# Optimization experiments

Measured on AMD Instinct MI355X. Metric: run time of the kernel, lower is better.

Reference implementation:

```python
import jax, jax.numpy as jnp
import numpy as np

NEG_INF = -(2.0**32) + 1.0  # matches tf: -2**32 + 1


def _positional_encoding(seq_len, d_model):
    # sinusoidal PE exactly as in the module (sin on even cols, cos on odd cols)
    pos = np.arange(seq_len)[:, None].astype(np.float32)
    i = np.arange(d_model)[None, :]
    angle_rates = 1.0 / np.power(10000.0, 2 * (i // 2) / np.float32(d_model))
    ang = pos * angle_rates
    ang[:, 0::2] = np.sin(ang[:, 0::2])
    ang[:, 1::2] = np.cos(ang[:, 1::2])
    return jnp.asarray(ang[None, ...], dtype=jnp.float32)  # [1, S, D]


def setup_inputs() -> dict:
    key = jax.random.key(0)
    kq, kk, kv, kw, km = jax.random.split(key, 5)
    B, S, D = 64, 512, 256
    q = jax.random.normal(kq, (B, S, D), dtype=jnp.float32)
    k = jax.random.normal(kk, (B, S, D), dtype=jnp.float32)
    v = jax.random.normal(kv, (B, S, D), dtype=jnp.float32)
    # keras 'random_uniform' initializer default range is [-0.05, 0.05]
    W = jax.random.uniform(kw, (D, D), dtype=jnp.float32, minval=-0.05, maxval=0.05)
    mask = jax.random.randint(km, (B, S), 0, 2, dtype=jnp.int32)
    return {"q": q, "k": k, "v": v, "W": W, "mask": mask}


def reference(q, k, v, W, mask):
    B, S, D = q.shape
    pe = _positional_encoding(S, D)  # [1, S, D]
    q = q + pe
    k = k + pe
    q = jax.nn.relu(jnp.einsum('bsd,de->bse', q, W))
    k = jax.nn.relu(jnp.einsum('bsd,de->bse', k, W))
    logits = jnp.einsum('bqd,bkd->bqk', q, k) / jnp.sqrt(jnp.float32(D))  # [B,S,S]
    # mask over key positions, broadcast across query dim
    logits = jnp.where(mask[:, None, :] == 0, jnp.float32(NEG_INF), logits)
    att = jax.nn.softmax(logits, axis=-1)
    out = jnp.einsum('bqk,bkd->bqd', att, v)
    return jnp.mean(out, axis=1)  # [B, D]
```

## Files before the change

### kernel.cpp

```cpp
#include <hip/hip_runtime.h>

#define NEG_INF (-4294967295.0f)

typedef _Float16 f16;
typedef _Float16 f16x8 __attribute__((ext_vector_type(8)));
typedef _Float16 f16x4v __attribute__((ext_vector_type(4)));
typedef float f32x4 __attribute__((ext_vector_type(4)));

#define MFMA16(a,b,c) __builtin_amdgcn_mfma_f32_16x16x32_f16((a),(b),(c),0,0,0)

#if defined(__has_builtin)
#if __has_builtin(__builtin_amdgcn_global_load_lds)
#define HAS_GLD 1
#endif
#endif

__device__ __forceinline__ void stage16(const void* g, void* lds_base, int lane) {
#ifdef HAS_GLD
    __builtin_amdgcn_global_load_lds(
        (const __attribute__((address_space(1))) unsigned int*)g,
        (__attribute__((address_space(3))) unsigned int*)lds_base, 16, 0, 0);
#else
    ((f16x8*)lds_base)[lane] = *(const f16x8*)g;
#endif
}

__global__ __launch_bounds__(256) void setup_kernel(const float* __restrict__ W,
                                                    float* __restrict__ pe,
                                                    f16* __restrict__ WT,
                                                    float* __restrict__ WG,
                                                    float* __restrict__ out) {
    const int bid = blockIdx.x, t = threadIdx.x;
    if (bid < 512) {
        int idx = bid * 256 + t;
        int s = idx >> 8, d = idx & 255;
        float x = (float)(d & ~1) * (1.f / 256.f);
        float rate = exp2f(x * -13.287712379549449f);
        float ang = (float)s * rate;
        pe[idx] = (d & 1) ? cosf(ang) : sinf(ang);
    } else if (bid < 768) {
        int e = bid - 512, d = t;
        WT[(e << 8) + d] = (f16)W[(d << 8) + e];
    } else if (bid == 768) {
        #pragma unroll
        for (int i = 0; i < 128; ++i) WG[i * 256 + t] = 0.f;
    } else {
        #pragma unroll
        for (int i = 0; i < 64; ++i) out[i * 256 + t] = 0.f;
    }
}

__global__ __launch_bounds__(1024, 4) void proj_kernel(const float* __restrict__ q,
                                                       const float* __restrict__ k,
                                                       const f16* __restrict__ WT,
                                                       const float* __restrict__ pe,
                                                       f16* __restrict__ outp) {
    __shared__ __align__(16) f16 lds[65536];
    f16* const As0 = lds;
    f16* const As1 = lds + 16384;
    f16* const Ws0 = lds + 32768;
    f16* const Ws1 = lds + 49152;

    const int t = threadIdx.x, l = t & 63, wv = t >> 6, lr = l & 15, lg = l >> 4;
    const int r0 = blockIdx.x * 256;
    const float* src = (r0 < 32768) ? q : k;
    const int rb = r0 & 32767;

    float4 av[4], pv[4];
    auto loadA = [&](int kc) {
        #pragma unroll
        for (int it = 0; it < 4; ++it) {
            int r = it * 64 + (t >> 4), d = (t & 15) * 4;
            av[it] = *(const float4*)(src + (size_t)(rb + r) * 256 + kc * 64 + d);
            pv[it] = *(const float4*)(pe + ((rb + r) & 511) * 256 + kc * 64 + d);
        }
    };
    auto writeA = [&](f16* dst) {
        #pragma unroll
        for (int it = 0; it < 4; ++it) {
            int r = it * 64 + (t >> 4), d = (t & 15) * 4;
            f16x4v h;
            h[0] = (f16)(av[it].x + pv[it].x); h[1] = (f16)(av[it].y + pv[it].y);
            h[2] = (f16)(av[it].z + pv[it].z); h[3] = (f16)(av[it].w + pv[it].w);
            *(f16x4v*)&dst[(r << 6) + (d ^ ((r & 7) << 3))] = h;
        }
    };
    auto stageW = [&](f16* dst, int kc) {
        #pragma unroll
        for (int it = 0; it < 2; ++it) {
            int eb = wv * 16 + it * 8;
            int e = eb + (l >> 3), c = l & 7;
            const f16* s = WT + (e << 8) + kc * 64 + ((c ^ (e & 7)) << 3);
            stage16(s, &dst[eb << 6], l);
        }
    };

    f32x4 acc[16] = {};
    loadA(0); stageW(Ws0, 0); writeA(As0);
    __syncthreads();

    #pragma unroll
    for (int kc = 0; kc < 4; ++kc) {
        f16* const Ac = (kc & 1) ? As1 : As0;
        f16* const Wc = (kc & 1) ? Ws1 : Ws0;
        f16* const An = (kc & 1) ? As0 : As1;
        f16* const Wn = (kc & 1) ? Ws0 : Ws1;
        if (kc < 3) { loadA(kc + 1); stageW(Wn, kc + 1); }
        #pragma unroll
        for (int kk = 0; kk < 2; ++kk) {
            int dk = kk * 32 + lg * 8;
            f16x8 a = *(const f16x8*)&Ac[((wv * 16 + lr) << 6) + (dk ^ ((lr & 7) << 3))];
            #pragma unroll
            for (int nt = 0; nt < 16; ++nt) {
                int e = nt * 16 + lr;
                f16x8 b = *(const f16x8*)&Wc[(e << 6) + (dk ^ ((lr & 7) << 3))];
                acc[nt] = MFMA16(a, b, acc[nt]);
            }
        }
        if (kc < 3) { writeA(An); __syncthreads(); }
    }

    __syncthreads();
    f16* Rb = lds + wv * 4096;
    #pragma unroll
    for (int nt = 0; nt < 16; ++nt) {
        #pragma unroll
        for (int rg = 0; rg < 4; ++rg) {
            int rr = lg * 4 + rg, col = nt * 16 + lr;
            float v = acc[nt][rg];
            v = v > 0.f ? v * 0.25f : 0.f;
            Rb[rr * 256 + ((((col >> 3) ^ (rr & 7)) << 3) | (col & 7))] = (f16)v;
        }
    }
    #pragma unroll
    for (int it = 0; it < 8; ++it) {
        int row = it * 2 + (l >> 5), c = l & 31;
        f16x8 v8 = *(const f16x8*)&Rb[row * 256 + ((c ^ (row & 7)) << 3)];
        *(f16x8*)(outp + (((size_t)(r0 + wv * 16 + row)) << 8) + c * 8) = v8;
    }
}

__global__ __launch_bounds__(256) void attn_kernel(const f16* __restrict__ QP,
                                                   const f16* __restrict__ KP,
                                                   const int* __restrict__ mask,
                                                   float* __restrict__ wglob) {
    __shared__ __align__(16) f16 Ks[2][32 * 256];
    __shared__ float ws[4][512];
    const int t = threadIdx.x, l = t & 63, wv = t >> 6, lr = l & 15, lg = l >> 4;
    const int n = blockIdx.x, bb = n & 63, qt = n >> 6;
    const int q0 = qt * 64 + wv * 16;
    const int* maskb = mask + bb * 512;

    auto stageK = [&](int dst, int kt) {
        #pragma unroll
        for (int it = 0; it < 4; ++it) {
            int r2 = wv * 8 + it * 2;
            int r = r2 + (l >> 5), c = l & 31;
            const f16* s = KP + (((size_t)(bb * 512 + kt * 32 + r)) << 8) + ((c ^ (r & 7)) << 3);
            stage16(s, &Ks[dst][r2 << 8], l);
        }
    };

    f16x8 qf[8];
    const f16* qrow = QP + (((size_t)(bb * 512 + q0 + lr)) << 8);
    #pragma unroll
    for (int kk = 0; kk < 8; ++kk) qf[kk] = *(const f16x8*)(qrow + kk * 32 + lg * 8);

    unsigned mb0 = 0, mb1 = 0;
    #pragma unroll
    for (int kt = 0; kt < 16; ++kt) {
        mb0 |= (maskb[kt * 32 + lr] ? 1u : 0u) << kt;
        mb1 |= (maskb[kt * 32 + 16 + lr] ? 1u : 0u) << kt;
    }

    float lacc[4] = {0.f, 0.f, 0.f, 0.f};
    f16 Pst[16][8];

    stageK(0, 0);
    __syncthreads();

    #pragma unroll
    for (int kt = 0; kt < 16; ++kt) {
        const int cur = kt & 1;
        if (kt < 15) stageK(cur ^ 1, kt + 1);
        f32x4 s0 = {}, s1 = {};
        #pragma unroll
        for (int kk = 0; kk < 8; ++kk) {
            int dk = kk * 32 + lg * 8;
            f16x8 b0 = *(const f16x8*)&Ks[cur][(lr << 8) + (dk ^ ((lr & 7) << 3))];
            f16x8 b1 = *(const f16x8*)&Ks[cur][((16 + lr) << 8) + (dk ^ ((lr & 7) << 3))];
            s0 = MFMA16(qf[kk], b0, s0);
            s1 = MFMA16(qf[kk], b1, s1);
        }
        #pragma unroll
        for (int rg = 0; rg < 4; ++rg) {
            float p0 = __expf(((mb0 >> kt) & 1) ? s0[rg] : NEG_INF);
            float p1 = __expf(((mb1 >> kt) & 1) ? s1[rg] : NEG_INF);
            f16 h0 = (f16)p0, h1 = (f16)p1;
            Pst[kt][rg] = h0;
            Pst[kt][4 + rg] = h1;
            lacc[rg] += (float)h0 + (float)h1;
        }
        if (kt < 15) __syncthreads();
    }

    #pragma unroll
    for (int rg = 0; rg < 4; ++rg) {
        float s = lacc[rg];
        s += __shfl_xor(s, 1); s += __shfl_xor(s, 2);
        s += __shfl_xor(s, 4); s += __shfl_xor(s, 8);
        lacc[rg] = s;
    }
    float rl[4];
    float bsum = 0.f;
    #pragma unroll
    for (int rg = 0; rg < 4; ++rg) {
        if (lacc[rg] > 0.f) { rl[rg] = 1.0f / lacc[rg]; }
        else                { rl[rg] = 0.f; bsum += 1.f / 512.f; }
    }

    #pragma unroll
    for (int kt = 0; kt < 16; ++kt) {
        float w0 = (float)Pst[kt][0] * rl[0] + (float)Pst[kt][1] * rl[1]
                 + (float)Pst[kt][2] * rl[2] + (float)Pst[kt][3] * rl[3] + bsum;
        float w1 = (float)Pst[kt][4] * rl[0] + (float)Pst[kt][5] * rl[1]
                 + (float)Pst[kt][6] * rl[2] + (float)Pst[kt][7] * rl[3] + bsum;
        w0 += __shfl_xor(w0, 16); w0 += __shfl_xor(w0, 32);
        w1 += __shfl_xor(w1, 16); w1 += __shfl_xor(w1, 32);
        if (lg == 0) {
            ws[wv][kt * 32 + lr] = w0;
            ws[wv][kt * 32 + 16 + lr] = w1;
        }
    }
    __syncthreads();
    #pragma unroll
    for (int i = 0; i < 2; ++i) {
        int kk = t + i * 256;
        float s = ws[0][kk] + ws[1][kk] + ws[2][kk] + ws[3][kk];
        atomicAdd(&wglob[bb * 512 + kk], s);
    }
}

__global__ __launch_bounds__(256) void wv_kernel(const float* __restrict__ wglob,
                                                 const float* __restrict__ V,
                                                 float* __restrict__ out) {
    const int n = blockIdx.x, bb = n & 63, ks = n >> 6;
    const int d = threadIdx.x;
    const float* wr = wglob + bb * 512 + ks * 64;
    const float* vb = V + ((((size_t)bb) * 512 + ks * 64) << 8) + d;
    float acc = 0.f;
    #pragma unroll 8
    for (int kk = 0; kk < 64; ++kk) acc = fmaf(wr[kk], vb[(size_t)kk << 8], acc);
    atomicAdd(&out[bb * 256 + d], acc * (1.f / 512.f));
}

extern "C" void kernel_launch(void* const* d_in, const int* in_sizes, int n_in,
                              void* d_out, int out_size, void* d_ws, size_t ws_size,
                              hipStream_t stream) {
    const float* q  = (const float*)d_in[0];
    const float* k  = (const float*)d_in[1];
    const float* v  = (const float*)d_in[2];
    const float* W  = (const float*)d_in[3];
    const int* mask = (const int*)d_in[4];

    char* ws = (char*)d_ws;
    f16*   QP = (f16*)ws;
    f16*   KP = (f16*)(ws + 16777216);
    float* PE = (float*)(ws + 33554432);
    f16*   WT = (f16*)(ws + 34078720);
    float* WG = (float*)(ws + 34209792);

    setup_kernel<<<770, 256, 0, stream>>>(W, PE, WT, WG, (float*)d_out);
    proj_kernel<<<256, 1024, 0, stream>>>(q, k, WT, PE, QP);
    attn_kernel<<<512, 256, 0, stream>>>(QP, KP, mask, WG);
    wv_kernel<<<512, 256, 0, stream>>>(WG, v, (float*)d_out);
}
```

Measured before the change: 175.9 us.

## Shrink projection blocks and keep A fragments in registers instead of LDS

The projection kernel moves from 1024-thread blocks covering 256 rows to 256-thread blocks covering 64 rows, launched as 1024 blocks. Each wave now loads its 16 input rows plus positional encoding straight into f16 register fragments for the whole K dimension. Only W is staged through a single 32 KB LDS buffer, replacing the earlier double-buffered A and W tiles. The aim is to cut LDS use and per-block size so more blocks fit per CU and more work runs in parallel. The cost is losing the double-buffered overlap of W loads (there is now a sync before and after each chunk), W being re-staged four times as often across the grid, and higher register pressure from the eight A fragments.

```diff
diff --git a/kernel.cpp b/kernel.cpp
--- a/kernel.cpp
+++ b/kernel.cpp
@@ -4,7 +4,6 @@
 
 typedef _Float16 f16;
 typedef _Float16 f16x8 __attribute__((ext_vector_type(8)));
-typedef _Float16 f16x4v __attribute__((ext_vector_type(4)));
 typedef float f32x4 __attribute__((ext_vector_type(4)));
 
 #define MFMA16(a,b,c) __builtin_amdgcn_mfma_f32_16x16x32_f16((a),(b),(c),0,0,0)
@@ -50,78 +49,61 @@
     }
 }
 
-__global__ __launch_bounds__(1024, 4) void proj_kernel(const float* __restrict__ q,
-                                                       const float* __restrict__ k,
-                                                       const f16* __restrict__ WT,
-                                                       const float* __restrict__ pe,
-                                                       f16* __restrict__ outp) {
-    __shared__ __align__(16) f16 lds[65536];
-    f16* const As0 = lds;
-    f16* const As1 = lds + 16384;
-    f16* const Ws0 = lds + 32768;
-    f16* const Ws1 = lds + 49152;
-
+__global__ __launch_bounds__(256, 4) void proj_kernel(const float* __restrict__ q,
+                                                      const float* __restrict__ k,
+                                                      const f16* __restrict__ WT,
+                                                      const float* __restrict__ pe,
+                                                      f16* __restrict__ outp) {
+    __shared__ __align__(16) f16 Ws[256 * 64];
     const int t = threadIdx.x, l = t & 63, wv = t >> 6, lr = l & 15, lg = l >> 4;
-    const int r0 = blockIdx.x * 256;
+    const int r0 = blockIdx.x * 64;
     const float* src = (r0 < 32768) ? q : k;
     const int rb = r0 & 32767;
 
-    float4 av[4], pv[4];
-    auto loadA = [&](int kc) {
-        #pragma unroll
-        for (int it = 0; it < 4; ++it) {
-            int r = it * 64 + (t >> 4), d = (t & 15) * 4;
-            av[it] = *(const float4*)(src + (size_t)(rb + r) * 256 + kc * 64 + d);
-            pv[it] = *(const float4*)(pe + ((rb + r) & 511) * 256 + kc * 64 + d);
-        }
-    };
-    auto writeA = [&](f16* dst) {
-        #pragma unroll
-        for (int it = 0; it < 4; ++it) {
-            int r = it * 64 + (t >> 4), d = (t & 15) * 4;
-            f16x4v h;
-            h[0] = (f16)(av[it].x + pv[it].x); h[1] = (f16)(av[it].y + pv[it].y);
-            h[2] = (f16)(av[it].z + pv[it].z); h[3] = (f16)(av[it].w + pv[it].w);
-            *(f16x4v*)&dst[(r << 6) + (d ^ ((r & 7) << 3))] = h;
-        }
-    };
-    auto stageW = [&](f16* dst, int kc) {
-        #pragma unroll
-        for (int it = 0; it < 2; ++it) {
-            int eb = wv * 16 + it * 8;
+    const float* arow = src + (size_t)(rb + wv * 16 + lr) * 256;
+    const float* prow = pe + (size_t)((rb + wv * 16 + lr) & 511) * 256;
+    f16x8 af[8];
+    #pragma unroll
+    for (int kk = 0; kk < 8; ++kk) {
+        int d = kk * 32 + lg * 8;
+        float4 a0 = *(const float4*)(arow + d);
+        float4 a1 = *(const float4*)(arow + d + 4);
+        float4 p0 = *(const float4*)(prow + d);
+        float4 p1 = *(const float4*)(prow + d + 4);
+        f16x8 h;
+        h[0] = (f16)(a0.x + p0.x); h[1] = (f16)(a0.y + p0.y);
+        h[2] = (f16)(a0.z + p0.z); h[3] = (f16)(a0.w + p0.w);
+        h[4] = (f16)(a1.x + p1.x); h[5] = (f16)(a1.y + p1.y);
+        h[6] = (f16)(a1.z + p1.z); h[7] = (f16)(a1.w + p1.w);
+        af[kk] = h;
+    }
+
+    f32x4 acc[16] = {};
+    #pragma unroll
+    for (int kc = 0; kc < 4; ++kc) {
+        #pragma unroll
+        for (int it = 0; it < 8; ++it) {
+            int eb = wv * 64 + it * 8;
             int e = eb + (l >> 3), c = l & 7;
             const f16* s = WT + (e << 8) + kc * 64 + ((c ^ (e & 7)) << 3);
-            stage16(s, &dst[eb << 6], l);
-        }
-    };
-
-    f32x4 acc[16] = {};
-    loadA(0); stageW(Ws0, 0); writeA(As0);
-    __syncthreads();
-
-    #pragma unroll
-    for (int kc = 0; kc < 4; ++kc) {
-        f16* const Ac = (kc & 1) ? As1 : As0;
-        f16* const Wc = (kc & 1) ? Ws1 : Ws0;
-        f16* const An = (kc & 1) ? As0 : As1;
-        f16* const Wn = (kc & 1) ? Ws0 : Ws1;
-        if (kc < 3) { loadA(kc + 1); stageW(Wn, kc + 1); }
+            stage16(s, &Ws[eb << 6], l);
+        }
+        __syncthreads();
         #pragma unroll
         for (int kk = 0; kk < 2; ++kk) {
             int dk = kk * 32 + lg * 8;
-            f16x8 a = *(const f16x8*)&Ac[((wv * 16 + lr) << 6) + (dk ^ ((lr & 7) << 3))];
+            f16x8 a = af[kc * 2 + kk];
             #pragma unroll
             for (int nt = 0; nt < 16; ++nt) {
                 int e = nt * 16 + lr;
-                f16x8 b = *(const f16x8*)&Wc[(e << 6) + (dk ^ ((lr & 7) << 3))];
+                f16x8 b = *(const f16x8*)&Ws[(e << 6) + (dk ^ ((lr & 7) << 3))];
                 acc[nt] = MFMA16(a, b, acc[nt]);
             }
         }
-        if (kc < 3) { writeA(An); __syncthreads(); }
-    }
-
-    __syncthreads();
-    f16* Rb = lds + wv * 4096;
+        __syncthreads();
+    }
+
+    f16* Rb = Ws + wv * 4096;
     #pragma unroll
     for (int nt = 0; nt < 16; ++nt) {
         #pragma unroll
@@ -271,7 +253,7 @@
     float* WG = (float*)(ws + 34209792);
 
     setup_kernel<<<770, 256, 0, stream>>>(W, PE, WT, WG, (float*)d_out);
-    proj_kernel<<<256, 1024, 0, stream>>>(q, k, WT, PE, QP);
+    proj_kernel<<<1024, 256, 0, stream>>>(q, k, WT, PE, QP);
     attn_kernel<<<512, 256, 0, stream>>>(QP, KP, mask, WG);
     wv_kernel<<<512, 256, 0, stream>>>(WG, v, (float*)d_out);
 }
```

Result: faster. 170.2 us (-3.3%).
